# Performance work log

Hardware: AMD Instinct MI355X
Metric: run time of the kernel (lower is better)

The kernel has to match this reference:

```python
import jax, jax.numpy as jnp
import numpy as np

V, E, H, M = 50000, 256, 512, 100   # vocab, emb_dim, hid_dim, mlp_hid_dim
H2 = H // 2                          # per-direction GRU size
B, S, T = 64, 400, 25                # batch, src_len, max_trg_len
EOS = 2                              # vocab['</s>'] -> CE weight 0


def _gru(x, h, Wih, Whh, bih, bhh):
    # torch GRU/GRUCell gate math
    gi = x @ Wih.T + bih
    gh = h @ Whh.T + bhh
    ir, iz, inn = jnp.split(gi, 3, axis=-1)
    hr, hz, hn = jnp.split(gh, 3, axis=-1)
    r = jax.nn.sigmoid(ir + hr)
    z = jax.nn.sigmoid(iz + hz)
    n = jnp.tanh(inn + r * hn)
    return (1.0 - z) * n + z * h


def _run_gru(xs, Wih, Whh, bih, bhh, reverse):
    # xs: [S, B, E] -> ys [S, B, H2], hT [B, H2]
    if reverse:
        xs = xs[::-1]
    h0 = jnp.zeros((xs.shape[1], Whh.shape[1]), xs.dtype)
    def step(h, x):
        h2 = _gru(x, h, Wih, Whh, bih, bhh)
        return h2, h2
    hT, ys = jax.lax.scan(step, h0, xs)
    if reverse:
        ys = ys[::-1]
    return ys, hT


def _model(src, trg, params):
    (emb, Wih_f, Whh_f, bih_f, bhh_f, Wih_b, Whh_b, bih_b, bhh_b,
     W1, b1, W2, b2, Wd, bd, We, be, Wo, bo,
     Wih_c, Whh_c, bih_c, bhh_c, Wv, bv) = params
    # ---- encode ----
    embeds = emb[src].transpose(1, 0, 2)                    # [S, B, E]
    ys_f, hf = _run_gru(embeds, Wih_f, Whh_f, bih_f, bhh_f, False)
    ys_b, hb = _run_gru(embeds, Wih_b, Whh_b, bih_b, bhh_b, True)
    states = jnp.concatenate([ys_f, ys_b], axis=-1)         # [S, B, H]
    enc_hidden = jnp.concatenate([hf, hb], axis=-1)         # [B, H]
    sgate = jax.nn.sigmoid(states @ W1.T + b1 + (enc_hidden @ W2.T + b2)[None])
    states = states * sgate
    enc_proj = states @ We.T + be                           # [S, B, M] (loop-invariant)
    # ---- decode (training path, weighted CE per step) ----
    def dec_step(carry, tok):
        h, loss = carry
        wemb = emb[tok]                                     # [B, E]
        e = jnp.tanh((h @ Wd.T + bd)[None] + enc_proj) @ Wo.T + bo  # [S, B, 1]
        a = jax.nn.softmax(e, axis=0)
        c = jnp.sum(a * states, axis=0)                     # [B, H]
        h2 = _gru(jnp.concatenate([c, wemb], axis=-1), h, Wih_c, Whh_c, bih_c, bhh_c)
        logits = h2 @ Wv.T + bv                             # [B, V]
        logp = jax.nn.log_softmax(logits, axis=-1)
        nll = -jnp.take_along_axis(logp, tok[:, None], axis=1)[:, 0]
        w = (tok != EOS).astype(logits.dtype)               # CE class weight mask
        step_loss = jnp.sum(w * nll) / jnp.sum(w)           # torch weighted-mean CE
        return (h2, loss + step_loss), None
    toks = trg[:, : T - 1].T                                # [T-1, B]
    (_, loss), _ = jax.lax.scan(dec_step, (enc_hidden, jnp.zeros((), states.dtype)), toks)
    return loss / B


def setup_inputs() -> dict:
    key = jax.random.key(0)
    ks = jax.random.split(key, 16)
    def p(k, shape, s=0.05):
        return jax.random.normal(k, shape, jnp.float32) * s
    z = lambda n: jnp.zeros((n,), jnp.float32)
    return {
        "src": jax.random.randint(ks[0], (B, S), 0, V, dtype=jnp.int32),
        "trg": jax.random.randint(ks[1], (B, T), 0, V, dtype=jnp.int32),
        "emb": p(ks[2], (V, E)),
        "Wih_f": p(ks[3], (3 * H2, E)), "Whh_f": p(ks[4], (3 * H2, H2)),
        "bih_f": z(3 * H2), "bhh_f": z(3 * H2),
        "Wih_b": p(ks[5], (3 * H2, E)), "Whh_b": p(ks[6], (3 * H2, H2)),
        "bih_b": z(3 * H2), "bhh_b": z(3 * H2),
        "W1": p(ks[7], (H, H)), "b1": z(H),
        "W2": p(ks[8], (H, H)), "b2": z(H),
        "Wd": p(ks[9], (M, H)), "bd": z(M),
        "We": p(ks[10], (M, H)), "be": z(M),
        "Wo": p(ks[11], (1, M)), "bo": z(1),
        "Wih_c": p(ks[12], (3 * H, H + E)), "Whh_c": p(ks[13], (3 * H, H)),
        "bih_c": z(3 * H), "bhh_c": z(3 * H),
        "Wv": p(ks[14], (V, H)), "bv": z(V),
    }


def reference(src, trg, emb, Wih_f, Whh_f, bih_f, bhh_f, Wih_b, Whh_b, bih_b, bhh_b,
              W1, b1, W2, b2, Wd, bd, We, be, Wo, bo,
              Wih_c, Whh_c, bih_c, bhh_c, Wv, bv):
    params = (emb, Wih_f, Whh_f, bih_f, bhh_f, Wih_b, Whh_b, bih_b, bhh_b,
              W1, b1, W2, b2, Wd, bd, We, be, Wo, bo,
              Wih_c, Whh_c, bih_c, bhh_c, Wv, bv)
    return _model(src, trg, params)
```

## Files before the change

### kernel.cpp

```cpp
#include <hip/hip_runtime.h>

typedef __bf16 bf16;
typedef bf16 bf16x2 __attribute__((ext_vector_type(2)));
typedef bf16 bf16x4 __attribute__((ext_vector_type(4)));
typedef bf16 bf16x8 __attribute__((ext_vector_type(8)));
typedef float f32x4 __attribute__((ext_vector_type(4)));

#define DEVFN __device__ __forceinline__

constexpr int cV = 50000, cE = 256, cH = 512, cM = 100, cH2 = 256;
constexpr int cB = 64, cS = 400, cT = 25, cEOS = 2;
constexpr int cSB = cS * cB;
constexpr int cG2 = 3 * cH2;
constexpr int cGP = 772;
constexpr int cKcat = 1280;
constexpr int cN4 = 2048;
constexpr int cNTV = (cV + 63) / 64;
constexpr int cTD = cT - 1;
constexpr int cVT = cV / 16;

constexpr size_t OFF_WV = 0;
constexpr size_t N_WV = (size_t)cV * cH;
constexpr size_t OFF_WIHF = OFF_WV + N_WV;
constexpr size_t N_WIH = (size_t)cG2 * cE;
constexpr size_t OFF_WHHF = OFF_WIHF + N_WIH;
constexpr size_t N_WHH = (size_t)cG2 * cH2;
constexpr size_t OFF_WIHB = OFF_WHHF + N_WHH;
constexpr size_t OFF_WHHB = OFF_WIHB + N_WIH;
constexpr size_t OFF_W1 = OFF_WHHB + N_WHH;
constexpr size_t N_WSQ = (size_t)cH * cH;
constexpr size_t OFF_W2 = OFF_W1 + N_WSQ;
constexpr size_t OFF_WE = OFF_W2 + N_WSQ;
constexpr size_t N_WE = (size_t)cM * cH;
constexpr size_t TOT_W = OFF_WE + N_WE;

struct GArgs {
  const bf16* A; const bf16* Bw; const float* bias;
  float* outF; bf16* outBf;
  const float* auxF; const bf16* auxBf;
  int M, N, K, ldo;
};

DEVFN float sigm(float x) { return 1.f / (1.f + __expf(-x)); }
DEVFN float tanh_f(float x) {
  float e2 = __expf(2.f * x);
  return 1.f - 2.f / (e2 + 1.f);
}

DEVFN void gload_lds16(const void* g, void* l) {
  __builtin_amdgcn_global_load_lds(
      (const __attribute__((address_space(1))) void*)g,
      (__attribute__((address_space(3))) void*)l, 16, 0, 0);
}

template <int EPI>
__global__ __launch_bounds__(256) void gemm64_k(GArgs g) {
  const int tid = threadIdx.x;
  const int w = blockIdx.x * 4 + (tid >> 6);
  const int tM = g.M >> 6;
  const int tN = (g.N + 63) >> 6;
  if (w >= tM * tN) return;
  const int im = w % tM, in = w / tM;
  const int m0 = im << 6, n0 = in << 6;
  const int lane = tid & 63, lr = lane & 15, lh = lane >> 4;

  f32x4 acc[4][4];
#pragma unroll
  for (int i = 0; i < 4; ++i)
#pragma unroll
    for (int j = 0; j < 4; ++j)
#pragma unroll
      for (int r = 0; r < 4; ++r) acc[i][j][r] = 0.f;

  bf16x8 bz;
#pragma unroll
  for (int q = 0; q < 8; ++q) bz[q] = (bf16)0.f;

  const int K = g.K;
#pragma unroll 2
  for (int k0 = 0; k0 < K; k0 += 32) {
    bf16x8 av[4], bw[4];
#pragma unroll
    for (int mt = 0; mt < 4; ++mt)
      av[mt] = *(const bf16x8*)(g.A + (size_t)(m0 + mt * 16 + lr) * K + k0 + lh * 8);
#pragma unroll
    for (int nt = 0; nt < 4; ++nt) {
      int row = n0 + nt * 16 + lr;
      bw[nt] = (row < g.N) ? *(const bf16x8*)(g.Bw + (size_t)row * K + k0 + lh * 8) : bz;
    }
#pragma unroll
    for (int mt = 0; mt < 4; ++mt)
#pragma unroll
      for (int nt = 0; nt < 4; ++nt)
        acc[mt][nt] = __builtin_amdgcn_mfma_f32_16x16x32_bf16(av[mt], bw[nt], acc[mt][nt], 0, 0, 0);
  }

  if constexpr (EPI == 4) {
#pragma unroll
    for (int mt = 0; mt < 4; ++mt)
#pragma unroll
      for (int nt = 0; nt < 4; ++nt) {
        const int n = n0 + nt * 16 + lr;
        if (n < g.N) {
          const float bia = g.bias[n];
#pragma unroll
          for (int r = 0; r < 4; ++r) {
            const int m = m0 + mt * 16 + lh * 4 + r;
            const int bb = m & 63, s = m >> 6;
            g.outF[((size_t)bb * cM + n) * cS + s] = acc[mt][nt][r] + bia;
          }
        }
      }
  } else {
#pragma unroll
    for (int mt = 0; mt < 4; ++mt) {
#pragma unroll
      for (int nt = 0; nt < 4; ++nt) {
        const int n = n0 + nt * 16 + lr;
        if (n < g.N) {
          const float bia = g.bias[n];
#pragma unroll
          for (int r = 0; r < 4; ++r) {
            const int m = m0 + mt * 16 + lh * 4 + r;
            float v = acc[mt][nt][r] + bia;
            if constexpr (EPI == 0) {
              g.outF[(size_t)m * g.ldo + n] = v;
            } else {
              float sg = sigm(v + g.auxF[(size_t)(m & 63) * g.ldo + n]);
              float st = (float)g.auxBf[(size_t)m * g.ldo + n];
              g.outBf[(size_t)m * g.ldo + n] = (bf16)(sg * st);
            }
          }
        }
      }
    }
  }
}

__global__ void cvt8_k(const float* __restrict__ wv, const float* __restrict__ wihf,
                       const float* __restrict__ whhf, const float* __restrict__ wihb,
                       const float* __restrict__ whhb, const float* __restrict__ w1,
                       const float* __restrict__ w2, const float* __restrict__ we,
                       bf16* __restrict__ dst) {
  size_t i = ((size_t)blockIdx.x * 256 + threadIdx.x) * 4;
  if (i >= TOT_W) return;
  if (i < OFF_WIHF) {
    float4 v = *(const float4*)(wv + i);
    size_t row = i >> 9, col = i & 511;
    size_t tile = row >> 4, lr = row & 15, kc = col >> 5, lh = (col >> 3) & 3, e = col & 7;
    size_t d = ((tile * 16 + kc) * 64 + lr * 4 + lh) * 8 + e;
    bf16x4 o;
    o[0] = (bf16)v.x; o[1] = (bf16)v.y; o[2] = (bf16)v.z; o[3] = (bf16)v.w;
    *(bf16x4*)(dst + d) = o;
    return;
  }
  const float* s;
  size_t off;
  if (i < OFF_WHHF) { s = wihf; off = OFF_WIHF; }
  else if (i < OFF_WIHB) { s = whhf; off = OFF_WHHF; }
  else if (i < OFF_WHHB) { s = wihb; off = OFF_WIHB; }
  else if (i < OFF_W1) { s = whhb; off = OFF_WHHB; }
  else if (i < OFF_W2) { s = w1; off = OFF_W1; }
  else if (i < OFF_WE) { s = w2; off = OFF_W2; }
  else { s = we; off = OFF_WE; }
  float4 v = *(const float4*)(s + (i - off));
  bf16x4 o;
  o[0] = (bf16)v.x; o[1] = (bf16)v.y; o[2] = (bf16)v.z; o[3] = (bf16)v.w;
  *(bf16x4*)(dst + i) = o;
}

__global__ void gather_k(const int* __restrict__ src, const float* __restrict__ emb,
                         bf16* __restrict__ embeds) {
  int i = blockIdx.x * 256 + threadIdx.x;
  int e = i & 255;
  int sb = i >> 8;
  int s = sb >> 6, b = sb & 63;
  int tok = src[b * cS + s];
  embeds[i] = (bf16)emb[(size_t)tok * cE + e];
}

__global__ void build_wp_k(const float* __restrict__ Wih_c, const float* __restrict__ Whh_c,
                           const float* __restrict__ bih_c, const float* __restrict__ bhh_c,
                           bf16* __restrict__ Wp, float* __restrict__ bp) {
  int i = blockIdx.x * 256 + threadIdx.x;
  if (i >= cN4 * cKcat) return;
  int j = i / cKcat, c = i % cKcat;
  int bi = j >> 6, gg = (j >> 4) & 3, idx = j & 15;
  int u = bi * 16 + idx;
  float v;
  if (gg == 0) v = (c < 768) ? Wih_c[(size_t)u * 768 + c] : Whh_c[(size_t)u * 512 + (c - 768)];
  else if (gg == 1) v = (c < 768) ? Wih_c[(size_t)(512 + u) * 768 + c] : Whh_c[(size_t)(512 + u) * 512 + (c - 768)];
  else if (gg == 2) v = (c < 768) ? Wih_c[(size_t)(1024 + u) * 768 + c] : 0.f;
  else v = (c < 768) ? 0.f : Whh_c[(size_t)(1024 + u) * 512 + (c - 768)];
  {
    size_t tile = (size_t)j >> 4, lr = j & 15, kc = c >> 5, lh = (c >> 3) & 3, e = c & 7;
    Wp[((tile * 40 + kc) * 64 + lr * 4 + lh) * 8 + e] = (bf16)v;
  }
  if (c == 0) {
    float bb;
    if (gg == 0) bb = bih_c[u] + bhh_c[u];
    else if (gg == 1) bb = bih_c[512 + u] + bhh_c[512 + u];
    else if (gg == 2) bb = bih_c[1024 + u];
    else bb = bhh_c[1024 + u];
    bp[j] = bb;
  }
}

__global__ void concat_k(const float* __restrict__ hf, const float* __restrict__ hb,
                         bf16* __restrict__ hd_bf, float* __restrict__ hd_f) {
  int i = blockIdx.x * 256 + threadIdx.x;
  if (i >= cB * cH) return;
  int b = i >> 9, k = i & 511;
  float v = (k < 256) ? hf[b * 256 + k] : hb[b * 256 + (k - 256)];
  hd_bf[i] = (bf16)v;
  hd_f[i] = v;
}

__global__ __launch_bounds__(256) void transp_k(const bf16* __restrict__ sg,
                                                bf16* __restrict__ sgT) {
  const int b = blockIdx.x, tid = threadIdx.x;
  __shared__ bf16 tile[64][520];
  for (int s0 = 0; s0 < cS; s0 += 64) {
    __syncthreads();
    for (int c = tid; c < 64 * 64; c += 256) {
      int row = c >> 6, col = c & 63;
      *(bf16x8*)(&tile[row][col * 8]) =
          *(const bf16x8*)(sg + ((size_t)(s0 + row) * cB + b) * cH + col * 8);
    }
    __syncthreads();
    for (int c = tid; c < 512 * 8; c += 256) {
      int k = c >> 3, sc = c & 7;
      bf16x8 v;
#pragma unroll
      for (int j = 0; j < 8; ++j) v[j] = tile[sc * 8 + j][k];
      *(bf16x8*)(sgT + ((size_t)b * cH + k) * cS + s0 + sc * 8) = v;
    }
  }
}

__global__ __launch_bounds__(512, 1) void enc_rnn_k(
    const bf16* __restrict__ WhhF, const bf16* __restrict__ WhhB,
    const float* __restrict__ giF, const float* __restrict__ giB,
    const float* __restrict__ bhhF, const float* __restrict__ bhhB,
    float* __restrict__ hfin, bf16* __restrict__ states) {
  const int blk = blockIdx.x;
  const int dir = blk >> 2;
  const int bc = blk & 3;
  const bf16* Whh = dir ? WhhB : WhhF;
  const float* gi = dir ? giB : giF;
  const float* bhh = dir ? bhhB : bhhF;

  const int tid = threadIdx.x;
  const int lane = tid & 63, w = tid >> 6;
  const int lr = lane & 15, lh = lane >> 4;
  const int u0 = w * 32;

  bf16x8 Bf[6][8];
  float bh[6];
#pragma unroll
  for (int gg = 0; gg < 3; ++gg)
#pragma unroll
    for (int ut = 0; ut < 2; ++ut) {
      int nbase = gg * 256 + u0 + ut * 16;
#pragma unroll
      for (int kf = 0; kf < 8; ++kf)
        Bf[gg * 2 + ut][kf] = *(const bf16x8*)(Whh + (size_t)(nbase + lr) * 256 + kf * 32 + lh * 8);
      bh[gg * 2 + ut] = bhh[nbase + lr];
    }

  __shared__ float gilds[2][16][cGP];
  __shared__ bf16 hs[2][16][264];

  auto prefetch = [&](int t2) {
    if (t2 >= cS) return;
    const int s2 = dir ? (cS - 1 - t2) : t2;
    const int buf = t2 & 1;
#pragma unroll
    for (int rr2 = 0; rr2 < 2; ++rr2) {
      const int row = w * 2 + rr2;
      const char* srcb = (const char*)(gi + ((size_t)s2 * cB + bc * 16 + row) * cG2);
      char* dstb = (char*)&gilds[buf][row][0];
#pragma unroll
      for (int c = 0; c < 3; ++c)
        gload_lds16(srcb + c * 1024 + lane * 16, dstb + c * 1024);
    }
  };

  float hreg[2][4];
#pragma unroll
  for (int ut = 0; ut < 2; ++ut)
#pragma unroll
    for (int r = 0; r < 4; ++r) hreg[ut][r] = 0.f;

  prefetch(0);
  for (int i = tid; i < 16 * 264; i += 512) ((bf16*)hs[0])[i] = (bf16)0.f;
  __syncthreads();

  for (int t = 0; t < cS; ++t) {
    const int buf = t & 1, nbuf = buf ^ 1;
    prefetch(t + 1);

    bf16x8 av[8];
#pragma unroll
    for (int kf = 0; kf < 8; ++kf)
      av[kf] = *(const bf16x8*)(&hs[buf][lr][kf * 32 + lh * 8]);

    float gir[2][4], giz[2][4], gin[2][4];
#pragma unroll
    for (int ut = 0; ut < 2; ++ut) {
      const int u = u0 + ut * 16 + lr;
#pragma unroll
      for (int r = 0; r < 4; ++r) {
        const int b = lh * 4 + r;
        gir[ut][r] = gilds[buf][b][u];
        giz[ut][r] = gilds[buf][b][256 + u];
        gin[ut][r] = gilds[buf][b][512 + u];
      }
    }

    f32x4 acc[6];
#pragma unroll
    for (int j = 0; j < 6; ++j)
#pragma unroll
      for (int r = 0; r < 4; ++r) acc[j][r] = 0.f;

#pragma unroll
    for (int kf = 0; kf < 8; ++kf)
#pragma unroll
      for (int nt = 0; nt < 6; ++nt)
        acc[nt] = __builtin_amdgcn_mfma_f32_16x16x32_bf16(av[kf], Bf[nt][kf], acc[nt], 0, 0, 0);

#pragma unroll
    for (int ut = 0; ut < 2; ++ut) {
      const int u = u0 + ut * 16 + lr;
#pragma unroll
      for (int r = 0; r < 4; ++r) {
        const int b = lh * 4 + r;
        float rr = sigm(gir[ut][r] + acc[ut][r] + bh[ut]);
        float zz = sigm(giz[ut][r] + acc[2 + ut][r] + bh[2 + ut]);
        float nn = tanh_f(gin[ut][r] + rr * (acc[4 + ut][r] + bh[4 + ut]));
        float hnew = (1.f - zz) * nn + zz * hreg[ut][r];
        hreg[ut][r] = hnew;
        hs[nbuf][b][u] = (bf16)hnew;
      }
    }

    __syncthreads();

    {
      const int s_src = dir ? (cS - 1 - t) : t;
      const int row = tid >> 5, c8 = tid & 31;
      bf16x8 v = *(const bf16x8*)(&hs[nbuf][row][c8 * 8]);
      *(bf16x8*)(states + ((size_t)s_src * cB + bc * 16 + row) * cH + dir * 256 + c8 * 8) = v;
    }
  }

#pragma unroll
  for (int ut = 0; ut < 2; ++ut)
#pragma unroll
    for (int r = 0; r < 4; ++r)
      hfin[((size_t)dir * cB + bc * 16 + lh * 4 + r) * cH2 + u0 + ut * 16 + lr] = hreg[ut][r];
}

__global__ __launch_bounds__(256) void attn_k(
    const bf16* __restrict__ hin, const float* __restrict__ Wd, const float* __restrict__ bd,
    const float* __restrict__ Wo, const float* __restrict__ bo,
    const float* __restrict__ epT, const bf16* __restrict__ sgT,
    const float* __restrict__ emb, const int* __restrict__ trg, int t,
    bf16* __restrict__ xh) {
  const int b = blockIdx.x, tid = threadIdx.x;
  const int lane = tid & 63, wid = tid >> 6;
  __shared__ float hsh[512];
  __shared__ float dsh[100];
  __shared__ float esh[400];
  __shared__ float red[16];

  for (int k = tid; k < 512; k += 256) hsh[k] = (float)hin[b * 512 + k];
  __syncthreads();

  for (int jj = 0; jj < 25; ++jj) {
    const int j = wid * 25 + jj;
    const float* wr = Wd + (size_t)j * 512 + lane * 8;
    float a = 0.f;
#pragma unroll
    for (int q = 0; q < 8; ++q) a += wr[q] * hsh[lane * 8 + q];
#pragma unroll
    for (int m = 1; m < 64; m <<= 1) a += __shfl_xor(a, m);
    if (lane == 0) dsh[j] = a + bd[j];
  }
  __syncthreads();

  const float bo0 = bo[0];
  const float* ep0 = epT + (size_t)b * cM * cS;
  float e0, e1 = -3.4e38f;
  {
    const float* p = ep0 + tid;
    float a = bo0;
#pragma unroll 4
    for (int j = 0; j < 100; ++j) a += Wo[j] * tanh_f(dsh[j] + p[j * cS]);
    e0 = a;
  }
  if (tid < 144) {
    const float* p = ep0 + 256 + tid;
    float a = bo0;
#pragma unroll 4
    for (int j = 0; j < 100; ++j) a += Wo[j] * tanh_f(dsh[j] + p[j * cS]);
    e1 = a;
  }
  float mx = fmaxf(e0, e1);
#pragma unroll
  for (int msk = 1; msk < 64; msk <<= 1) mx = fmaxf(mx, __shfl_xor(mx, msk));
  if (lane == 0) red[wid] = mx;
  __syncthreads();
  mx = fmaxf(fmaxf(red[0], red[1]), fmaxf(red[2], red[3]));

  float a0 = __expf(e0 - mx);
  float a1 = (tid < 144) ? __expf(e1 - mx) : 0.f;
  esh[tid] = a0;
  if (tid < 144) esh[tid + 256] = a1;
  float sm = a0 + a1;
#pragma unroll
  for (int msk = 1; msk < 64; msk <<= 1) sm += __shfl_xor(sm, msk);
  if (lane == 0) red[8 + wid] = sm;
  __syncthreads();
  const float inv = 1.f / (red[8] + red[9] + red[10] + red[11]);

  {
    const bf16* sp0 = sgT + ((size_t)b * cH + tid) * cS;
    const bf16* sp1 = sp0 + (size_t)256 * cS;
    float c0 = 0.f, c1 = 0.f;
    for (int s = 0; s < cS; s += 8) {
      bf16x8 v0 = *(const bf16x8*)(sp0 + s);
      bf16x8 v1 = *(const bf16x8*)(sp1 + s);
#pragma unroll
      for (int j = 0; j < 8; ++j) {
        float wj = esh[s + j];
        c0 += wj * (float)v0[j];
        c1 += wj * (float)v1[j];
      }
    }
    xh[(size_t)b * cKcat + tid] = (bf16)(c0 * inv);
    xh[(size_t)b * cKcat + 256 + tid] = (bf16)(c1 * inv);
  }
  const int tok = trg[b * cT + t];
  xh[(size_t)b * cKcat + 512 + tid] = (bf16)emb[(size_t)tok * cE + tid];
  for (int k = tid; k < 512; k += 256) xh[(size_t)b * cKcat + 768 + k] = hin[b * 512 + k];
}

__global__ __launch_bounds__(256) void gru_k(
    const bf16* __restrict__ xh, const bf16* __restrict__ Wp, const float* __restrict__ bp,
    const float* __restrict__ hin_f, float* __restrict__ hout_f, bf16* __restrict__ hallt) {
  const int tid = threadIdx.x;
  const int lane = tid & 63, wid = tid >> 6;
  const int w = blockIdx.x * 4 + wid;
  const int n0 = w << 6, lr = lane & 15, lh = lane >> 4;
  f32x4 acc[4][4];
#pragma unroll
  for (int i = 0; i < 4; ++i)
#pragma unroll
    for (int j = 0; j < 4; ++j)
#pragma unroll
      for (int r = 0; r < 4; ++r) acc[i][j][r] = 0.f;
#pragma unroll 2
  for (int k0 = 0; k0 < cKcat; k0 += 32) {
    bf16x8 av[4], bw[4];
#pragma unroll
    for (int mt = 0; mt < 4; ++mt)
      av[mt] = *(const bf16x8*)(xh + (size_t)(mt * 16 + lr) * cKcat + k0 + lh * 8);
#pragma unroll
    for (int nt = 0; nt < 4; ++nt)
      bw[nt] = *(const bf16x8*)(Wp + (((size_t)(w * 4 + nt) * 40 + (k0 >> 5)) * 64 + lr * 4 + lh) * 8);
#pragma unroll
    for (int mt = 0; mt < 4; ++mt)
#pragma unroll
      for (int nt = 0; nt < 4; ++nt)
        acc[mt][nt] = __builtin_amdgcn_mfma_f32_16x16x32_bf16(av[mt], bw[nt], acc[mt][nt], 0, 0, 0);
  }
  const int u = (n0 >> 2) + lr;
  const float br = bp[n0 + lr];
  const float bz2 = bp[n0 + 16 + lr];
  const float bi2 = bp[n0 + 32 + lr];
  const float bh2 = bp[n0 + 48 + lr];
#pragma unroll
  for (int mt = 0; mt < 4; ++mt)
#pragma unroll
    for (int r = 0; r < 4; ++r) {
      const int bb = mt * 16 + lh * 4 + r;
      float rr = sigm(acc[mt][0][r] + br);
      float zz = sigm(acc[mt][1][r] + bz2);
      float nn = tanh_f(acc[mt][2][r] + bi2 + rr * (acc[mt][3][r] + bh2));
      float h2v = (1.f - zz) * nn + zz * hin_f[(size_t)bb * cH + u];
      hout_f[(size_t)bb * cH + u] = h2v;
      hallt[(size_t)bb * cH + u] = (bf16)h2v;
    }
}

__global__ __launch_bounds__(256) void biglogits_k(
    const bf16* __restrict__ hall, const bf16* __restrict__ WvS,
    const float* __restrict__ bv, float* __restrict__ partials) {
  const int tid = threadIdx.x;
  const int lane = tid & 63, wid = tid >> 6;
  const int im = blockIdx.x % cTD;
  const int in = (blockIdx.x / cTD) * 4 + wid;
  if (in >= cNTV) return;
  const int m0 = im << 6, lr = lane & 15, lh = lane >> 4;

  f32x4 acc[4][4];
#pragma unroll
  for (int i = 0; i < 4; ++i)
#pragma unroll
    for (int j = 0; j < 4; ++j)
#pragma unroll
      for (int r = 0; r < 4; ++r) acc[i][j][r] = 0.f;
  bf16x8 bz;
#pragma unroll
  for (int q = 0; q < 8; ++q) bz[q] = (bf16)0.f;

#pragma unroll 2
  for (int k0 = 0; k0 < cH; k0 += 32) {
    bf16x8 av[4], bw[4];
#pragma unroll
    for (int mt = 0; mt < 4; ++mt)
      av[mt] = *(const bf16x8*)(hall + (size_t)(m0 + mt * 16 + lr) * cH + k0 + lh * 8);
#pragma unroll
    for (int nt = 0; nt < 4; ++nt) {
      const int tile = in * 4 + nt;
      bw[nt] = (tile < cVT)
                   ? *(const bf16x8*)(WvS + (((size_t)tile * 16 + (k0 >> 5)) * 64 + lr * 4 + lh) * 8)
                   : bz;
    }
#pragma unroll
    for (int mt = 0; mt < 4; ++mt)
#pragma unroll
      for (int nt = 0; nt < 4; ++nt)
        acc[mt][nt] = __builtin_amdgcn_mfma_f32_16x16x32_bf16(av[mt], bw[nt], acc[mt][nt], 0, 0, 0);
  }

#pragma unroll
  for (int mt = 0; mt < 4; ++mt) {
#pragma unroll
    for (int r = 0; r < 4; ++r) {
      const int m = m0 + mt * 16 + lh * 4 + r;
      float vv[4];
      float mx = -3.4e38f;
#pragma unroll
      for (int nt = 0; nt < 4; ++nt) {
        int n = (in << 6) + nt * 16 + lr;
        float v = (n < cV) ? (acc[mt][nt][r] + bv[n]) : -3.4e38f;
        vv[nt] = v;
        mx = fmaxf(mx, v);
      }
#pragma unroll
      for (int msk = 1; msk < 16; msk <<= 1) mx = fmaxf(mx, __shfl_xor(mx, msk));
      float sm = 0.f;
#pragma unroll
      for (int nt = 0; nt < 4; ++nt) {
        int n = (in << 6) + nt * 16 + lr;
        if (n < cV) sm += __expf(vv[nt] - mx);
      }
#pragma unroll
      for (int msk = 1; msk < 16; msk <<= 1) sm += __shfl_xor(sm, msk);
      if (lr == 0) {
        float* p = partials + ((size_t)m * cNTV + in) * 2;
        p[0] = mx;
        p[1] = sm;
      }
    }
  }
}

__global__ __launch_bounds__(64) void rowloss_all_k(
    const float* __restrict__ partials, const bf16* __restrict__ hall,
    const float* __restrict__ Wv, const float* __restrict__ bv,
    const int* __restrict__ trg, float* __restrict__ rnll, float* __restrict__ rw) {
  const int m = blockIdx.x, tid = threadIdx.x;
  const int t = m >> 6, bb = m & 63;
  float mx = -3.4e38f, sm = 0.f;
  const float* pr = partials + (size_t)m * cNTV * 2;
  for (int p = tid; p < cNTV; p += 64) {
    float m2 = pr[p * 2], s2 = pr[p * 2 + 1];
    if (m2 > mx) { sm = sm * __expf(mx - m2) + s2; mx = m2; }
    else sm += s2 * __expf(m2 - mx);
  }
#pragma unroll
  for (int msk = 1; msk < 64; msk <<= 1) {
    float om = __shfl_xor(mx, msk), os = __shfl_xor(sm, msk);
    if (om > mx) { sm = sm * __expf(mx - om) + os; mx = om; }
    else sm += os * __expf(om - mx);
  }
  const int tok = trg[bb * cT + t];
  float dot = 0.f;
  {
    const float* wr = Wv + (size_t)tok * cH + tid * 8;
    const bf16* hr = hall + (size_t)m * cH + tid * 8;
    bf16x8 h8 = *(const bf16x8*)hr;
#pragma unroll
    for (int j = 0; j < 8; ++j) dot += (float)h8[j] * wr[j];
  }
#pragma unroll
  for (int msk = 1; msk < 64; msk <<= 1) dot += __shfl_xor(dot, msk);
  if (tid == 0) {
    float lse = mx + __logf(sm);
    float nll = lse - (dot + bv[tok]);
    float wgt = (tok != cEOS) ? 1.f : 0.f;
    rnll[m] = wgt * nll;
    rw[m] = wgt;
  }
}

__global__ __launch_bounds__(64) void final_loss_k(const float* __restrict__ rnll,
                                                   const float* __restrict__ rw,
                                                   float* __restrict__ out) {
  __shared__ float sl[32];
  const int t = threadIdx.x;
  if (t < cTD) {
    float a = 0.f, d = 0.f;
    for (int b = 0; b < cB; ++b) { a += rnll[t * cB + b]; d += rw[t * cB + b]; }
    sl[t] = a / d;
  }
  __syncthreads();
  if (t == 0) {
    float s = 0.f;
    for (int i = 0; i < cTD; ++i) s += sl[i];
    out[0] = s / (float)cB;
  }
}

extern "C" void kernel_launch(void* const* d_in, const int* in_sizes, int n_in,
                              void* d_out, int out_size, void* d_ws, size_t ws_size,
                              hipStream_t stream) {
  (void)in_sizes; (void)n_in; (void)out_size; (void)ws_size;
  const int* src = (const int*)d_in[0];
  const int* trg = (const int*)d_in[1];
  const float* emb = (const float*)d_in[2];
  const float* Wih_f = (const float*)d_in[3];
  const float* Whh_f = (const float*)d_in[4];
  const float* bih_f = (const float*)d_in[5];
  const float* bhh_f = (const float*)d_in[6];
  const float* Wih_b = (const float*)d_in[7];
  const float* Whh_b = (const float*)d_in[8];
  const float* bih_b = (const float*)d_in[9];
  const float* bhh_b = (const float*)d_in[10];
  const float* W1 = (const float*)d_in[11];
  const float* b1 = (const float*)d_in[12];
  const float* W2 = (const float*)d_in[13];
  const float* b2 = (const float*)d_in[14];
  const float* Wd = (const float*)d_in[15];
  const float* bd = (const float*)d_in[16];
  const float* We = (const float*)d_in[17];
  const float* be = (const float*)d_in[18];
  const float* Wo = (const float*)d_in[19];
  const float* bo = (const float*)d_in[20];
  const float* Wih_c = (const float*)d_in[21];
  const float* Whh_c = (const float*)d_in[22];
  const float* bih_c = (const float*)d_in[23];
  const float* bhh_c = (const float*)d_in[24];
  const float* Wv = (const float*)d_in[25];
  const float* bv = (const float*)d_in[26];
  float* out = (float*)d_out;

  char* ws = (char*)d_ws;
  size_t off = 0;
  auto carve = [&](size_t bytes) -> void* {
    void* p = ws + off;
    off += (bytes + 255) & ~(size_t)255;
    return p;
  };
  bf16* wcat = (bf16*)carve(TOT_W * 2);
  bf16* WvS = wcat + OFF_WV;
  bf16* Wihf_b = wcat + OFF_WIHF;
  bf16* Whhf_b = wcat + OFF_WHHF;
  bf16* Wihb_b = wcat + OFF_WIHB;
  bf16* Whhb_b = wcat + OFF_WHHB;
  bf16* W1_b = wcat + OFF_W1;
  bf16* W2_b = wcat + OFF_W2;
  bf16* We_b = wcat + OFF_WE;
  bf16* Wp_b = (bf16*)carve((size_t)cN4 * cKcat * 2);
  float* bp = (float*)carve((size_t)cN4 * 4);
  bf16* embeds = (bf16*)carve((size_t)cSB * cE * 2);
  float* gi_f = (float*)carve((size_t)cSB * cG2 * 4);
  float* gi_b = (float*)carve((size_t)cSB * cG2 * 4);
  bf16* states = (bf16*)carve((size_t)cSB * cH * 2);
  bf16* statesg = (bf16*)carve((size_t)cSB * cH * 2);
  bf16* statesgT = (bf16*)carve((size_t)cSB * cH * 2);
  float* hfin = (float*)carve((size_t)2 * cB * cH2 * 4);
  bf16* hdec0_bf = (bf16*)carve((size_t)cB * cH * 2);
  float* hdec0_f = (float*)carve((size_t)cB * cH * 4);
  float* hf0 = (float*)carve((size_t)cB * cH * 4);
  float* hf1 = (float*)carve((size_t)cB * cH * 4);
  float* hw2 = (float*)carve((size_t)cB * cH * 4);
  float* epT = (float*)carve((size_t)cB * cM * cS * 4);
  bf16* xh = (bf16*)carve((size_t)cB * cKcat * 2);
  bf16* hall = (bf16*)carve((size_t)cTD * cB * cH * 2);
  float* partials = (float*)carve((size_t)cTD * cB * cNTV * 2 * 4);
  float* rnll = (float*)carve((size_t)cTD * cB * 4);
  float* rw = (float*)carve((size_t)cTD * cB * 4);

  auto gemm0 = [&](const bf16* A, const bf16* Bm, const float* bias, float* outF,
                   int M, int N, int K, int ldo) {
    GArgs ga{A, Bm, bias, outF, nullptr, nullptr, nullptr, M, N, K, ldo};
    int waves = (M / 64) * ((N + 63) / 64);
    gemm64_k<0><<<dim3((waves + 3) / 4), dim3(256), 0, stream>>>(ga);
  };

  cvt8_k<<<dim3((TOT_W / 4 + 255) / 256), dim3(256), 0, stream>>>(
      Wv, Wih_f, Whh_f, Wih_b, Whh_b, W1, W2, We, wcat);
  build_wp_k<<<dim3((cN4 * cKcat + 255) / 256), dim3(256), 0, stream>>>(
      Wih_c, Whh_c, bih_c, bhh_c, Wp_b, bp);

  gather_k<<<dim3(cSB * cE / 256), dim3(256), 0, stream>>>(src, emb, embeds);
  gemm0(embeds, Wihf_b, bih_f, gi_f, cSB, cG2, cE, cG2);
  gemm0(embeds, Wihb_b, bih_b, gi_b, cSB, cG2, cE, cG2);
  enc_rnn_k<<<dim3(8), dim3(512), 0, stream>>>(Whhf_b, Whhb_b, gi_f, gi_b, bhh_f, bhh_b,
                                               hfin, states);
  concat_k<<<dim3((cB * cH + 255) / 256), dim3(256), 0, stream>>>(
      hfin, hfin + (size_t)cB * cH2, hdec0_bf, hdec0_f);
  gemm0(hdec0_bf, W2_b, b2, hw2, cB, cH, cH, cH);
  {
    GArgs ga{states, W1_b, b1, nullptr, statesg, hw2, states, cSB, cH, cH, cH};
    int waves = (cSB / 64) * (cH / 64);
    gemm64_k<1><<<dim3((waves + 3) / 4), dim3(256), 0, stream>>>(ga);
  }
  {
    GArgs ga{statesg, We_b, be, epT, nullptr, nullptr, nullptr, cSB, cM, cH, 0};
    int waves = (cSB / 64) * ((cM + 63) / 64);
    gemm64_k<4><<<dim3((waves + 3) / 4), dim3(256), 0, stream>>>(ga);
  }
  transp_k<<<dim3(cB), dim3(256), 0, stream>>>(statesg, statesgT);

  for (int t = 0; t < cTD; ++t) {
    const bf16* hin_bf = (t == 0) ? hdec0_bf : (hall + (size_t)(t - 1) * cB * cH);
    const float* hin_f = (t == 0) ? hdec0_f : ((t & 1) ? hf0 : hf1);
    float* hout_f = (t & 1) ? hf1 : hf0;

    attn_k<<<dim3(cB), dim3(256), 0, stream>>>(hin_bf, Wd, bd, Wo, bo, epT, statesgT,
                                               emb, trg, t, xh);
    gru_k<<<dim3(8), dim3(256), 0, stream>>>(xh, Wp_b, bp, hin_f, hout_f,
                                             hall + (size_t)t * cB * cH);
  }

  biglogits_k<<<dim3(cTD * ((cNTV + 3) / 4)), dim3(256), 0, stream>>>(hall, WvS, bv, partials);
  rowloss_all_k<<<dim3(cTD * cB), dim3(64), 0, stream>>>(partials, hall, Wv, bv, trg, rnll, rw);
  final_loss_k<<<dim3(1), dim3(64), 0, stream>>>(rnll, rw, out);
}
```

Before: 4.272 ms.

## Fuse decoder loop into persistent kernel overlapping vocab logits with recurrence

Replaces the 48 per-step attention/GRU launches and the separate vocab-logits kernel with one persistent 128-block kernel that uses global atomic barriers between phases. Blocks idle during the attention or GRU phase compute the logits tiles for the previous step's hidden state, so the large Wv GEMM is spread across the serial recurrence. This removes launch overhead and fills idle compute, at the cost of spin barriers, and it assumes all 128 blocks are co-resident. The previously parallel logits GEMM now runs on at most 128 blocks.

```diff
diff --git a/kernel.cpp b/kernel.cpp
--- a/kernel.cpp
+++ b/kernel.cpp
@@ -18,6 +18,7 @@
 constexpr int cNTV = (cV + 63) / 64;
 constexpr int cTD = cT - 1;
 constexpr int cVT = cV / 16;
+constexpr int cDB = 128;
 
 constexpr size_t OFF_WV = 0;
 constexpr size_t N_WV = (size_t)cV * cH;
@@ -169,6 +170,10 @@
   *(bf16x4*)(dst + i) = o;
 }
 
+__global__ void init_k(unsigned* bar) {
+  if (threadIdx.x < 64) bar[threadIdx.x] = 0u;
+}
+
 __global__ void gather_k(const int* __restrict__ src, const float* __restrict__ emb,
                          bf16* __restrict__ embeds) {
   int i = blockIdx.x * 256 + threadIdx.x;
@@ -362,149 +367,10 @@
       hfin[((size_t)dir * cB + bc * 16 + lh * 4 + r) * cH2 + u0 + ut * 16 + lr] = hreg[ut][r];
 }
 
-__global__ __launch_bounds__(256) void attn_k(
-    const bf16* __restrict__ hin, const float* __restrict__ Wd, const float* __restrict__ bd,
-    const float* __restrict__ Wo, const float* __restrict__ bo,
-    const float* __restrict__ epT, const bf16* __restrict__ sgT,
-    const float* __restrict__ emb, const int* __restrict__ trg, int t,
-    bf16* __restrict__ xh) {
-  const int b = blockIdx.x, tid = threadIdx.x;
-  const int lane = tid & 63, wid = tid >> 6;
-  __shared__ float hsh[512];
-  __shared__ float dsh[100];
-  __shared__ float esh[400];
-  __shared__ float red[16];
-
-  for (int k = tid; k < 512; k += 256) hsh[k] = (float)hin[b * 512 + k];
-  __syncthreads();
-
-  for (int jj = 0; jj < 25; ++jj) {
-    const int j = wid * 25 + jj;
-    const float* wr = Wd + (size_t)j * 512 + lane * 8;
-    float a = 0.f;
-#pragma unroll
-    for (int q = 0; q < 8; ++q) a += wr[q] * hsh[lane * 8 + q];
-#pragma unroll
-    for (int m = 1; m < 64; m <<= 1) a += __shfl_xor(a, m);
-    if (lane == 0) dsh[j] = a + bd[j];
-  }
-  __syncthreads();
-
-  const float bo0 = bo[0];
-  const float* ep0 = epT + (size_t)b * cM * cS;
-  float e0, e1 = -3.4e38f;
-  {
-    const float* p = ep0 + tid;
-    float a = bo0;
-#pragma unroll 4
-    for (int j = 0; j < 100; ++j) a += Wo[j] * tanh_f(dsh[j] + p[j * cS]);
-    e0 = a;
-  }
-  if (tid < 144) {
-    const float* p = ep0 + 256 + tid;
-    float a = bo0;
-#pragma unroll 4
-    for (int j = 0; j < 100; ++j) a += Wo[j] * tanh_f(dsh[j] + p[j * cS]);
-    e1 = a;
-  }
-  float mx = fmaxf(e0, e1);
-#pragma unroll
-  for (int msk = 1; msk < 64; msk <<= 1) mx = fmaxf(mx, __shfl_xor(mx, msk));
-  if (lane == 0) red[wid] = mx;
-  __syncthreads();
-  mx = fmaxf(fmaxf(red[0], red[1]), fmaxf(red[2], red[3]));
-
-  float a0 = __expf(e0 - mx);
-  float a1 = (tid < 144) ? __expf(e1 - mx) : 0.f;
-  esh[tid] = a0;
-  if (tid < 144) esh[tid + 256] = a1;
-  float sm = a0 + a1;
-#pragma unroll
-  for (int msk = 1; msk < 64; msk <<= 1) sm += __shfl_xor(sm, msk);
-  if (lane == 0) red[8 + wid] = sm;
-  __syncthreads();
-  const float inv = 1.f / (red[8] + red[9] + red[10] + red[11]);
-
-  {
-    const bf16* sp0 = sgT + ((size_t)b * cH + tid) * cS;
-    const bf16* sp1 = sp0 + (size_t)256 * cS;
-    float c0 = 0.f, c1 = 0.f;
-    for (int s = 0; s < cS; s += 8) {
-      bf16x8 v0 = *(const bf16x8*)(sp0 + s);
-      bf16x8 v1 = *(const bf16x8*)(sp1 + s);
-#pragma unroll
-      for (int j = 0; j < 8; ++j) {
-        float wj = esh[s + j];
-        c0 += wj * (float)v0[j];
-        c1 += wj * (float)v1[j];
-      }
-    }
-    xh[(size_t)b * cKcat + tid] = (bf16)(c0 * inv);
-    xh[(size_t)b * cKcat + 256 + tid] = (bf16)(c1 * inv);
-  }
-  const int tok = trg[b * cT + t];
-  xh[(size_t)b * cKcat + 512 + tid] = (bf16)emb[(size_t)tok * cE + tid];
-  for (int k = tid; k < 512; k += 256) xh[(size_t)b * cKcat + 768 + k] = hin[b * 512 + k];
-}
-
-__global__ __launch_bounds__(256) void gru_k(
-    const bf16* __restrict__ xh, const bf16* __restrict__ Wp, const float* __restrict__ bp,
-    const float* __restrict__ hin_f, float* __restrict__ hout_f, bf16* __restrict__ hallt) {
-  const int tid = threadIdx.x;
-  const int lane = tid & 63, wid = tid >> 6;
-  const int w = blockIdx.x * 4 + wid;
-  const int n0 = w << 6, lr = lane & 15, lh = lane >> 4;
-  f32x4 acc[4][4];
-#pragma unroll
-  for (int i = 0; i < 4; ++i)
-#pragma unroll
-    for (int j = 0; j < 4; ++j)
-#pragma unroll
-      for (int r = 0; r < 4; ++r) acc[i][j][r] = 0.f;
-#pragma unroll 2
-  for (int k0 = 0; k0 < cKcat; k0 += 32) {
-    bf16x8 av[4], bw[4];
-#pragma unroll
-    for (int mt = 0; mt < 4; ++mt)
-      av[mt] = *(const bf16x8*)(xh + (size_t)(mt * 16 + lr) * cKcat + k0 + lh * 8);
-#pragma unroll
-    for (int nt = 0; nt < 4; ++nt)
-      bw[nt] = *(const bf16x8*)(Wp + (((size_t)(w * 4 + nt) * 40 + (k0 >> 5)) * 64 + lr * 4 + lh) * 8);
-#pragma unroll
-    for (int mt = 0; mt < 4; ++mt)
-#pragma unroll
-      for (int nt = 0; nt < 4; ++nt)
-        acc[mt][nt] = __builtin_amdgcn_mfma_f32_16x16x32_bf16(av[mt], bw[nt], acc[mt][nt], 0, 0, 0);
-  }
-  const int u = (n0 >> 2) + lr;
-  const float br = bp[n0 + lr];
-  const float bz2 = bp[n0 + 16 + lr];
-  const float bi2 = bp[n0 + 32 + lr];
-  const float bh2 = bp[n0 + 48 + lr];
-#pragma unroll
-  for (int mt = 0; mt < 4; ++mt)
-#pragma unroll
-    for (int r = 0; r < 4; ++r) {
-      const int bb = mt * 16 + lh * 4 + r;
-      float rr = sigm(acc[mt][0][r] + br);
-      float zz = sigm(acc[mt][1][r] + bz2);
-      float nn = tanh_f(acc[mt][2][r] + bi2 + rr * (acc[mt][3][r] + bh2));
-      float h2v = (1.f - zz) * nn + zz * hin_f[(size_t)bb * cH + u];
-      hout_f[(size_t)bb * cH + u] = h2v;
-      hallt[(size_t)bb * cH + u] = (bf16)h2v;
-    }
-}
-
-__global__ __launch_bounds__(256) void biglogits_k(
-    const bf16* __restrict__ hall, const bf16* __restrict__ WvS,
-    const float* __restrict__ bv, float* __restrict__ partials) {
-  const int tid = threadIdx.x;
-  const int lane = tid & 63, wid = tid >> 6;
-  const int im = blockIdx.x % cTD;
-  const int in = (blockIdx.x / cTD) * 4 + wid;
-  if (in >= cNTV) return;
+DEVFN void logits_tile64(int im, int in, int lane, const bf16* __restrict__ hall,
+                         const bf16* __restrict__ WvS, const float* __restrict__ bv,
+                         float* __restrict__ partials) {
   const int m0 = im << 6, lr = lane & 15, lh = lane >> 4;
-
   f32x4 acc[4][4];
 #pragma unroll
   for (int i = 0; i < 4; ++i)
@@ -565,6 +431,190 @@
         p[0] = mx;
         p[1] = sm;
       }
+    }
+  }
+}
+
+__global__ __launch_bounds__(256, 1) void dec_loop_k(
+    const bf16* __restrict__ hdec0_bf, const float* __restrict__ hdec0_f,
+    const float* __restrict__ Wd, const float* __restrict__ bd,
+    const float* __restrict__ Wo, const float* __restrict__ bo,
+    const float* __restrict__ epT, const bf16* __restrict__ sgT,
+    const float* __restrict__ emb, const int* __restrict__ trg,
+    const bf16* __restrict__ Wp, const float* __restrict__ bp,
+    const bf16* __restrict__ WvS, const float* __restrict__ bv,
+    bf16* __restrict__ xh, bf16* __restrict__ hall,
+    float* __restrict__ hfA, float* __restrict__ hfB,
+    float* __restrict__ partials, unsigned* __restrict__ bar) {
+  const int blk = blockIdx.x, tid = threadIdx.x;
+  const int lane = tid & 63, wid = tid >> 6;
+
+  __shared__ float hsh[512];
+  __shared__ float dsh[100];
+  __shared__ float esh[400];
+  __shared__ float red[16];
+
+  auto barrier_at = [&](int ph) {
+    __threadfence();
+    __syncthreads();
+    if (tid == 0) {
+      __hip_atomic_fetch_add(&bar[ph], 1u, __ATOMIC_ACQ_REL, __HIP_MEMORY_SCOPE_AGENT);
+      while (__hip_atomic_load(&bar[ph], __ATOMIC_ACQUIRE, __HIP_MEMORY_SCOPE_AGENT) < (unsigned)cDB)
+        __builtin_amdgcn_s_sleep(2);
+    }
+    __syncthreads();
+    __threadfence();
+  };
+
+  for (int t = 0; t < cTD; ++t) {
+    const bf16* hin = (t == 0) ? hdec0_bf : (hall + (size_t)(t - 1) * cB * cH);
+
+    if (blk < cB) {
+      const int b = blk;
+      for (int k = tid; k < 512; k += 256) hsh[k] = (float)hin[b * 512 + k];
+      __syncthreads();
+
+      for (int jj = 0; jj < 25; ++jj) {
+        const int j = wid * 25 + jj;
+        const float* wr = Wd + (size_t)j * 512 + lane * 8;
+        float a = 0.f;
+#pragma unroll
+        for (int q = 0; q < 8; ++q) a += wr[q] * hsh[lane * 8 + q];
+#pragma unroll
+        for (int m = 1; m < 64; m <<= 1) a += __shfl_xor(a, m);
+        if (lane == 0) dsh[j] = a + bd[j];
+      }
+      __syncthreads();
+
+      const float bo0 = bo[0];
+      const float* ep0 = epT + (size_t)b * cM * cS;
+      float e0, e1 = -3.4e38f;
+      {
+        const float* p = ep0 + tid;
+        float a = bo0;
+#pragma unroll 4
+        for (int j = 0; j < 100; ++j) a += Wo[j] * tanh_f(dsh[j] + p[j * cS]);
+        e0 = a;
+      }
+      if (tid < 144) {
+        const float* p = ep0 + 256 + tid;
+        float a = bo0;
+#pragma unroll 4
+        for (int j = 0; j < 100; ++j) a += Wo[j] * tanh_f(dsh[j] + p[j * cS]);
+        e1 = a;
+      }
+      float mx = fmaxf(e0, e1);
+#pragma unroll
+      for (int msk = 1; msk < 64; msk <<= 1) mx = fmaxf(mx, __shfl_xor(mx, msk));
+      if (lane == 0) red[wid] = mx;
+      __syncthreads();
+      mx = fmaxf(fmaxf(red[0], red[1]), fmaxf(red[2], red[3]));
+
+      float a0 = __expf(e0 - mx);
+      float a1 = (tid < 144) ? __expf(e1 - mx) : 0.f;
+      esh[tid] = a0;
+      if (tid < 144) esh[tid + 256] = a1;
+      float sm = a0 + a1;
+#pragma unroll
+      for (int msk = 1; msk < 64; msk <<= 1) sm += __shfl_xor(sm, msk);
+      if (lane == 0) red[8 + wid] = sm;
+      __syncthreads();
+      const float inv = 1.f / (red[8] + red[9] + red[10] + red[11]);
+
+      {
+        const bf16* sp0 = sgT + ((size_t)b * cH + tid) * cS;
+        const bf16* sp1 = sp0 + (size_t)256 * cS;
+        float c0 = 0.f, c1 = 0.f;
+        for (int s = 0; s < cS; s += 8) {
+          bf16x8 v0 = *(const bf16x8*)(sp0 + s);
+          bf16x8 v1 = *(const bf16x8*)(sp1 + s);
+#pragma unroll
+          for (int j = 0; j < 8; ++j) {
+            float wj = esh[s + j];
+            c0 += wj * (float)v0[j];
+            c1 += wj * (float)v1[j];
+          }
+        }
+        xh[(size_t)b * cKcat + tid] = (bf16)(c0 * inv);
+        xh[(size_t)b * cKcat + 256 + tid] = (bf16)(c1 * inv);
+      }
+      const int tok = trg[b * cT + t];
+      xh[(size_t)b * cKcat + 512 + tid] = (bf16)emb[(size_t)tok * cE + tid];
+      for (int k = tid; k < 512; k += 256) xh[(size_t)b * cKcat + 768 + k] = hin[b * 512 + k];
+    } else if (t > 0) {
+      const int idx = blk - cB;
+#pragma unroll
+      for (int q = 0; q < 2; ++q) {
+        const int s = wid + 4 * q;
+        if (s < 7) {
+          const int in = idx * 7 + s;
+          if (in < cNTV) logits_tile64(t - 1, in, lane, hall, WvS, bv, partials);
+        }
+      }
+    }
+    barrier_at(2 * t);
+
+    if (blk < 8) {
+      const float* hin_f = (t == 0) ? hdec0_f : ((t & 1) ? hfA : hfB);
+      float* hout_f = (t & 1) ? hfB : hfA;
+      bf16* hallt = hall + (size_t)t * cB * cH;
+      const int w = blk * 4 + wid;
+      const int n0 = w << 6, lr = lane & 15, lh = lane >> 4;
+      f32x4 acc[4][4];
+#pragma unroll
+      for (int i = 0; i < 4; ++i)
+#pragma unroll
+        for (int j = 0; j < 4; ++j)
+#pragma unroll
+          for (int r = 0; r < 4; ++r) acc[i][j][r] = 0.f;
+#pragma unroll 2
+      for (int k0 = 0; k0 < cKcat; k0 += 32) {
+        bf16x8 av[4], bw[4];
+#pragma unroll
+        for (int mt = 0; mt < 4; ++mt)
+          av[mt] = *(const bf16x8*)(xh + (size_t)(mt * 16 + lr) * cKcat + k0 + lh * 8);
+#pragma unroll
+        for (int nt = 0; nt < 4; ++nt)
+          bw[nt] = *(const bf16x8*)(Wp + (((size_t)(w * 4 + nt) * 40 + (k0 >> 5)) * 64 + lr * 4 + lh) * 8);
+#pragma unroll
+        for (int mt = 0; mt < 4; ++mt)
+#pragma unroll
+          for (int nt = 0; nt < 4; ++nt)
+            acc[mt][nt] = __builtin_amdgcn_mfma_f32_16x16x32_bf16(av[mt], bw[nt], acc[mt][nt], 0, 0, 0);
+      }
+      const int u = (n0 >> 2) + lr;
+      const float br = bp[n0 + lr];
+      const float bz2 = bp[n0 + 16 + lr];
+      const float bi2 = bp[n0 + 32 + lr];
+      const float bh2 = bp[n0 + 48 + lr];
+#pragma unroll
+      for (int mt = 0; mt < 4; ++mt)
+#pragma unroll
+        for (int r = 0; r < 4; ++r) {
+          const int bb = mt * 16 + lh * 4 + r;
+          float rr = sigm(acc[mt][0][r] + br);
+          float zz = sigm(acc[mt][1][r] + bz2);
+          float nn = tanh_f(acc[mt][2][r] + bi2 + rr * (acc[mt][3][r] + bh2));
+          float h2v = (1.f - zz) * nn + zz * hin_f[(size_t)bb * cH + u];
+          hout_f[(size_t)bb * cH + u] = h2v;
+          hallt[(size_t)bb * cH + u] = (bf16)h2v;
+        }
+    } else if (t > 0) {
+      const int idx = blk - 8;
+      if (wid < 3) {
+        const int in = 448 + idx * 3 + wid;
+        if (in < cNTV) logits_tile64(t - 1, in, lane, hall, WvS, bv, partials);
+      }
+    }
+    barrier_at(2 * t + 1);
+  }
+
+  {
+    const int slot = blk * 4 + wid;
+#pragma unroll
+    for (int q = 0; q < 2; ++q) {
+      const int in = slot + 512 * q;
+      if (in < cNTV) logits_tile64(cTD - 1, in, lane, hall, WvS, bv, partials);
     }
   }
 }
@@ -686,8 +736,8 @@
   float* hfin = (float*)carve((size_t)2 * cB * cH2 * 4);
   bf16* hdec0_bf = (bf16*)carve((size_t)cB * cH * 2);
   float* hdec0_f = (float*)carve((size_t)cB * cH * 4);
-  float* hf0 = (float*)carve((size_t)cB * cH * 4);
-  float* hf1 = (float*)carve((size_t)cB * cH * 4);
+  float* hfA = (float*)carve((size_t)cB * cH * 4);
+  float* hfB = (float*)carve((size_t)cB * cH * 4);
   float* hw2 = (float*)carve((size_t)cB * cH * 4);
   float* epT = (float*)carve((size_t)cB * cM * cS * 4);
   bf16* xh = (bf16*)carve((size_t)cB * cKcat * 2);
@@ -695,6 +745,7 @@
   float* partials = (float*)carve((size_t)cTD * cB * cNTV * 2 * 4);
   float* rnll = (float*)carve((size_t)cTD * cB * 4);
   float* rw = (float*)carve((size_t)cTD * cB * 4);
+  unsigned* bar = (unsigned*)carve(64 * 4);
 
   auto gemm0 = [&](const bf16* A, const bf16* Bm, const float* bias, float* outF,
                    int M, int N, int K, int ldo) {
@@ -703,6 +754,7 @@
     gemm64_k<0><<<dim3((waves + 3) / 4), dim3(256), 0, stream>>>(ga);
   };
 
+  init_k<<<dim3(1), dim3(64), 0, stream>>>(bar);
   cvt8_k<<<dim3((TOT_W / 4 + 255) / 256), dim3(256), 0, stream>>>(
       Wv, Wih_f, Whh_f, Wih_b, Whh_b, W1, W2, We, wcat);
   build_wp_k<<<dim3((cN4 * cKcat + 255) / 256), dim3(256), 0, stream>>>(
@@ -728,18 +780,10 @@
   }
   transp_k<<<dim3(cB), dim3(256), 0, stream>>>(statesg, statesgT);
 
-  for (int t = 0; t < cTD; ++t) {
-    const bf16* hin_bf = (t == 0) ? hdec0_bf : (hall + (size_t)(t - 1) * cB * cH);
-    const float* hin_f = (t == 0) ? hdec0_f : ((t & 1) ? hf0 : hf1);
-    float* hout_f = (t & 1) ? hf1 : hf0;
-
-    attn_k<<<dim3(cB), dim3(256), 0, stream>>>(hin_bf, Wd, bd, Wo, bo, epT, statesgT,
-                                               emb, trg, t, xh);
-    gru_k<<<dim3(8), dim3(256), 0, stream>>>(xh, Wp_b, bp, hin_f, hout_f,
-                                             hall + (size_t)t * cB * cH);
-  }
-
-  biglogits_k<<<dim3(cTD * ((cNTV + 3) / 4)), dim3(256), 0, stream>>>(hall, WvS, bv, partials);
+  dec_loop_k<<<dim3(cDB), dim3(256), 0, stream>>>(
+      hdec0_bf, hdec0_f, Wd, bd, Wo, bo, epT, statesgT, emb, trg,
+      Wp_b, bp, WvS, bv, xh, hall, hfA, hfB, partials, bar);
+
   rowloss_all_k<<<dim3(cTD * cB), dim3(64), 0, stream>>>(partials, hall, Wv, bv, trg, rnll, rw);
   final_loss_k<<<dim3(1), dim3(64), 0, stream>>>(rnll, rw, out);
 }
```

Measured after the change: 6.211 ms. 1.45x slower.
